# Optimization experiments

Hardware: AMD Instinct MI355X
Metric: run time of the kernel (lower is better)

The kernel has to match this reference:

```python
import jax, jax.numpy as jnp
import numpy as np

HORIZONTAL = 4
VERTICAL = 4


def _laplacian3(x):
    """kornia.filters.laplacian(x, kernel_size=3): 3x3 all-ones kernel with
    center -8, normalized by sum(|k|)=16, reflect padding, depthwise conv.
    x: [B, C, H, W] -> [B, C, H, W]."""
    C = x.shape[1]
    k = np.ones((3, 3), dtype=np.float32)
    k[1, 1] = -8.0
    k /= 16.0  # kornia normalized=True
    kern = jnp.asarray(k, dtype=x.dtype)[None, None].repeat(C, axis=0)  # [C,1,3,3]
    xp = jnp.pad(x, ((0, 0), (0, 0), (1, 1), (1, 1)), mode="reflect")
    return jax.lax.conv_general_dilated(
        xp, kern, window_strides=(1, 1), padding="VALID",
        dimension_numbers=("NCHW", "OIHW", "NCHW"), feature_group_count=C)


def setup_inputs() -> dict:
    key = jax.random.key(0)
    k1, k2 = jax.random.split(key)
    shape = (32, 3, 512, 512)
    return {
        "ground_truth_batch": jax.random.normal(k1, shape, dtype=jnp.float32),
        "segmented_print_batch": jax.random.normal(k2, shape, dtype=jnp.float32),
    }


def reference(ground_truth_batch, segmented_print_batch):
    gt_grad = _laplacian3(ground_truth_batch)
    sp_grad = _laplacian3(segmented_print_batch)
    diff = jnp.abs(gt_grad - sp_grad)  # L1, reduction='sum' per block
    B, C, H, W = diff.shape
    vb, hb = H // VERTICAL, W // HORIZONTAL
    # Original code does image.reshape([H, W, C]) (flat reinterpret), then
    # sums |diff| over [vb, hb, C] blocks of that view. Reproduce exactly:
    d = diff.reshape(B, H, W, C)
    blocks = d.reshape(B, VERTICAL, vb, HORIZONTAL, hb, C).sum(axis=(2, 4, 5))  # [B, V, Hz]
    # Per image, keep the max-loss block; total loss = sum over batch.
    return jnp.max(blocks, axis=(1, 2)).sum()
```

## Files before the change

### kernel.cpp

```cpp
#include <hip/hip_runtime.h>

#define HH 512
#define WW 512
#define CC 3
#define BANDS 8
#define ROWS_PER_BAND 64


__global__ void zero_blocks_kernel(float* __restrict__ blocks, int n) {
    int i = blockIdx.x * blockDim.x + threadIdx.x;
    if (i < n) blocks[i] = 0.0f;
}

__global__ __launch_bounds__(256) void lap_block_sum_kernel(
    const float* __restrict__ gt, const float* __restrict__ sp,
    float* __restrict__ blocks)
{
    __shared__ float ring[4][WW];
    __shared__ float red[4][4];

    const int band = blockIdx.x;
    const int c    = blockIdx.y;
    const int b    = blockIdx.z;
    const int t    = threadIdx.x;
    const int w0   = 2 * t;
    const int w1   = w0 + 1;

    const int h0 = band * ROWS_PER_BAND;
    const size_t plane = (size_t)(b * CC + c) * (size_t)(HH * WW);
    const float* __restrict__ gtp = gt + plane;
    const float* __restrict__ spp = sp + plane;

    auto load_row = [&](int hr) {
        int hs = hr < 0 ? 1 : (hr > HH - 1 ? HH - 2 : hr);
        const float2 g = *(const float2*)(gtp + (size_t)hs * WW + w0);
        const float2 s = *(const float2*)(spp + (size_t)hs * WW + w0);
        float2 d = make_float2(g.x - s.x, g.y - s.y);
        *(float2*)&ring[hr & 3][w0] = d;
    };

    load_row(h0 - 1);
    load_row(h0);

    const int fr0 = c * HH + h0;
    const int v   = fr0 / 384;
    const int hz_m0 = (0 * 512 + w0) / 384;
    const int hz_m1 = (1 * 512 + w0) / 384;
    const int hz_m2 = (2 * 512 + w0) / 384;

    const int wm1 = (w0 == 0)      ? 1      : w0 - 1;
    const int wp2 = (w1 == WW - 1) ? WW - 2 : w1 + 1;

    float acc0 = 0.0f, acc1 = 0.0f, acc2 = 0.0f, acc3 = 0.0f;

    int m = fr0 % 3;
    #pragma unroll 4
    for (int h = h0; h < h0 + ROWS_PER_BAND; ++h) {
        load_row(h + 1);
        __syncthreads();
        const float* __restrict__ r0 = ring[(h - 1) & 3];
        const float* __restrict__ r1 = ring[h & 3];
        const float* __restrict__ r2 = ring[(h + 1) & 3];

        float cm  = r0[wm1] + r1[wm1] + r2[wm1];
        float c0v = r1[w0];
        float cs0 = r0[w0] + c0v + r2[w0];
        float c1v = r1[w1];
        float cs1 = r0[w1] + c1v + r2[w1];
        float cp  = r0[wp2] + r1[wp2] + r2[wp2];

        float lap0 = (cm  + cs0 + cs1 - 9.0f * c0v) * 0.0625f;
        float lap1 = (cs0 + cs1 + cp  - 9.0f * c1v) * 0.0625f;
        float s = fabsf(lap0) + fabsf(lap1);

        int hz = (m == 0) ? hz_m0 : ((m == 1) ? hz_m1 : hz_m2);
        acc0 += (hz == 0) ? s : 0.0f;
        acc1 += (hz == 1) ? s : 0.0f;
        acc2 += (hz == 2) ? s : 0.0f;
        acc3 += (hz == 3) ? s : 0.0f;

        m = (m == 2) ? 0 : m + 1;
    }

    #pragma unroll
    for (int off = 32; off > 0; off >>= 1) {
        acc0 += __shfl_xor(acc0, off);
        acc1 += __shfl_xor(acc1, off);
        acc2 += __shfl_xor(acc2, off);
        acc3 += __shfl_xor(acc3, off);
    }
    const int wave = t >> 6;
    const int lane = t & 63;
    if (lane == 0) {
        red[wave][0] = acc0; red[wave][1] = acc1;
        red[wave][2] = acc2; red[wave][3] = acc3;
    }
    __syncthreads();
    if (t < 4) {
        float r = red[0][t] + red[1][t] + red[2][t] + red[3][t];
        atomicAdd(&blocks[(b * 4 + v) * 4 + t], r);
    }
}

__global__ void finalize_kernel(const float* __restrict__ blocks,
                                float* __restrict__ out, int B) {
    int t = threadIdx.x;
    float m = 0.0f;
    if (t < B) {
        m = blocks[t * 16];
        #pragma unroll
        for (int i = 1; i < 16; ++i) m = fmaxf(m, blocks[t * 16 + i]);
    }
    #pragma unroll
    for (int off = 16; off > 0; off >>= 1) m += __shfl_down(m, off, 32);
    if (t == 0) out[0] = m;
}

extern "C" void kernel_launch(void* const* d_in, const int* in_sizes, int n_in,
                              void* d_out, int out_size, void* d_ws, size_t ws_size,
                              hipStream_t stream) {
    const float* gt = (const float*)d_in[0];
    const float* sp = (const float*)d_in[1];
    float* blocks = (float*)d_ws;
    float* out = (float*)d_out;

    const int B = in_sizes[0] / (CC * HH * WW);

    zero_blocks_kernel<<<1, 512, 0, stream>>>(blocks, B * 16);

    dim3 grid(BANDS, CC, B);
    lap_block_sum_kernel<<<grid, 256, 0, stream>>>(gt, sp, blocks);

    finalize_kernel<<<1, 64, 0, stream>>>(blocks, out, B);
}
```

Baseline: 45.44 us.

## Register-resident stencil with wave-independent row strips and atomic-free partials

Replaces the shared-memory row ring buffer and its per-row __syncthreads with a register sliding window. Each wave owns 8 rows and handles 4-wide columns loaded as float4, with horizontal neighbours fetched by lane shuffles. The grid doubles to 16 bands, and atomics plus the zeroing kernel are replaced by per-workgroup partial sums that a larger finalize kernel reduces. This removes LDS traffic, block-level sync and one launch. In exchange each wave reloads 2 halo rows per 8-row strip and register pressure rises.

Result: slower. 131.0 us (+188.2%).

```diff
diff --git a/kernel.cpp b/kernel.cpp
--- a/kernel.cpp
+++ b/kernel.cpp
@@ -3,84 +3,102 @@
 #define HH 512
 #define WW 512
 #define CC 3
-#define BANDS 8
-#define ROWS_PER_BAND 64
+#define BANDS 16
+#define BAND_ROWS 32
+#define RPW 8
 
 
-__global__ void zero_blocks_kernel(float* __restrict__ blocks, int n) {
-    int i = blockIdx.x * blockDim.x + threadIdx.x;
-    if (i < n) blocks[i] = 0.0f;
-}
-
-__global__ __launch_bounds__(256) void lap_block_sum_kernel(
+__global__ __launch_bounds__(256, 5) void lap_block_sum_kernel(
     const float* __restrict__ gt, const float* __restrict__ sp,
-    float* __restrict__ blocks)
+    float* __restrict__ partial)
 {
-    __shared__ float ring[4][WW];
     __shared__ float red[4][4];
 
-    const int band = blockIdx.x;
-    const int c    = blockIdx.y;
-    const int b    = blockIdx.z;
-    const int t    = threadIdx.x;
-    const int w0   = 2 * t;
-    const int w1   = w0 + 1;
+    const int band = blockIdx.x, c = blockIdx.y, b = blockIdx.z;
+    const int t = threadIdx.x;
+    const int wv = t >> 6, lane = t & 63;
 
-    const int h0 = band * ROWS_PER_BAND;
     const size_t plane = (size_t)(b * CC + c) * (size_t)(HH * WW);
     const float* __restrict__ gtp = gt + plane;
     const float* __restrict__ spp = sp + plane;
 
-    auto load_row = [&](int hr) {
-        int hs = hr < 0 ? 1 : (hr > HH - 1 ? HH - 2 : hr);
-        const float2 g = *(const float2*)(gtp + (size_t)hs * WW + w0);
-        const float2 s = *(const float2*)(spp + (size_t)hs * WW + w0);
-        float2 d = make_float2(g.x - s.x, g.y - s.y);
-        *(float2*)&ring[hr & 3][w0] = d;
-    };
+    const int h0   = band * BAND_ROWS + wv * RPW;
+    const int colA = 4 * lane;
+    const int colB = 256 + 4 * lane;
 
-    load_row(h0 - 1);
-    load_row(h0);
+    const int hzA_0 = (colA) / 384, hzA_1 = (512 + colA) / 384, hzA_2 = (1024 + colA) / 384;
+    const int hzB_0 = (colB) / 384, hzB_1 = (512 + colB) / 384, hzB_2 = (1024 + colB) / 384;
 
-    const int fr0 = c * HH + h0;
-    const int v   = fr0 / 384;
-    const int hz_m0 = (0 * 512 + w0) / 384;
-    const int hz_m1 = (1 * 512 + w0) / 384;
-    const int hz_m2 = (2 * 512 + w0) / 384;
+    float dA[3][4], dB[3][4];
+    float lnA[3], rnA[3], lnB[3], rnB[3];
 
-    const int wm1 = (w0 == 0)      ? 1      : w0 - 1;
-    const int wp2 = (w1 == WW - 1) ? WW - 2 : w1 + 1;
+#define LOAD_ROW(HR, S) do {                                                  \
+        int hs_ = (HR); hs_ = hs_ < 0 ? 1 : (hs_ > HH - 1 ? HH - 2 : hs_);    \
+        const float* gr_ = gtp + (size_t)hs_ * WW;                            \
+        const float* sr_ = spp + (size_t)hs_ * WW;                            \
+        float4 ga_ = *(const float4*)(gr_ + colA);                            \
+        float4 gb_ = *(const float4*)(gr_ + colB);                            \
+        float4 sa_ = *(const float4*)(sr_ + colA);                            \
+        float4 sb_ = *(const float4*)(sr_ + colB);                            \
+        dA[S][0] = ga_.x - sa_.x; dA[S][1] = ga_.y - sa_.y;                   \
+        dA[S][2] = ga_.z - sa_.z; dA[S][3] = ga_.w - sa_.w;                   \
+        dB[S][0] = gb_.x - sb_.x; dB[S][1] = gb_.y - sb_.y;                   \
+        dB[S][2] = gb_.z - sb_.z; dB[S][3] = gb_.w - sb_.w;                   \
+        float lA_  = __shfl(dA[S][3], lane - 1);                              \
+        float rA_  = __shfl(dA[S][0], lane + 1);                              \
+        float lB_  = __shfl(dB[S][3], lane - 1);                              \
+        float rB_  = __shfl(dB[S][0], lane + 1);                              \
+        float xAB_ = __shfl(dB[S][0], 0);      \
+        float xBA_ = __shfl(dA[S][3], 63);      \
+        lnA[S] = (lane == 0)  ? dA[S][1] : lA_;      \
+        rnA[S] = (lane == 63) ? xAB_     : rA_;                               \
+        lnB[S] = (lane == 0)  ? xBA_     : lB_;                               \
+        rnB[S] = (lane == 63) ? dB[S][2] : rB_;   \
+    } while (0)
 
-    float acc0 = 0.0f, acc1 = 0.0f, acc2 = 0.0f, acc3 = 0.0f;
+    LOAD_ROW(h0 - 1, 0);
+    LOAD_ROW(h0,     1);
 
-    int m = fr0 % 3;
-    #pragma unroll 4
-    for (int h = h0; h < h0 + ROWS_PER_BAND; ++h) {
-        load_row(h + 1);
-        __syncthreads();
-        const float* __restrict__ r0 = ring[(h - 1) & 3];
-        const float* __restrict__ r1 = ring[h & 3];
-        const float* __restrict__ r2 = ring[(h + 1) & 3];
+    float acc0 = 0.f, acc1 = 0.f, acc2 = 0.f, acc3 = 0.f;
+    int m = (c * HH + h0) % 3;
 
-        float cm  = r0[wm1] + r1[wm1] + r2[wm1];
-        float c0v = r1[w0];
-        float cs0 = r0[w0] + c0v + r2[w0];
-        float c1v = r1[w1];
-        float cs1 = r0[w1] + c1v + r2[w1];
-        float cp  = r0[wp2] + r1[wp2] + r2[wp2];
+    #pragma unroll
+    for (int i = 0; i < RPW; ++i) {
+        const int sB_ = (i + 2) % 3, sT = i % 3, sM = (i + 1) % 3;
+        LOAD_ROW(h0 + i + 1, sB_);
 
-        float lap0 = (cm  + cs0 + cs1 - 9.0f * c0v) * 0.0625f;
-        float lap1 = (cs0 + cs1 + cp  - 9.0f * c1v) * 0.0625f;
-        float s = fabsf(lap0) + fabsf(lap1);
+        float csA0 = dA[sT][0] + dA[sM][0] + dA[sB_][0];
+        float csA1 = dA[sT][1] + dA[sM][1] + dA[sB_][1];
+        float csA2 = dA[sT][2] + dA[sM][2] + dA[sB_][2];
+        float csA3 = dA[sT][3] + dA[sM][3] + dA[sB_][3];
+        float csLA = lnA[sT] + lnA[sM] + lnA[sB_];
+        float csRA = rnA[sT] + rnA[sM] + rnA[sB_];
+        float sA = fabsf(csLA + csA0 + csA1 - 9.f * dA[sM][0])
+                 + fabsf(csA0 + csA1 + csA2 - 9.f * dA[sM][1])
+                 + fabsf(csA1 + csA2 + csA3 - 9.f * dA[sM][2])
+                 + fabsf(csA2 + csA3 + csRA - 9.f * dA[sM][3]);
 
-        int hz = (m == 0) ? hz_m0 : ((m == 1) ? hz_m1 : hz_m2);
-        acc0 += (hz == 0) ? s : 0.0f;
-        acc1 += (hz == 1) ? s : 0.0f;
-        acc2 += (hz == 2) ? s : 0.0f;
-        acc3 += (hz == 3) ? s : 0.0f;
+        float csB0 = dB[sT][0] + dB[sM][0] + dB[sB_][0];
+        float csB1 = dB[sT][1] + dB[sM][1] + dB[sB_][1];
+        float csB2 = dB[sT][2] + dB[sM][2] + dB[sB_][2];
+        float csB3 = dB[sT][3] + dB[sM][3] + dB[sB_][3];
+        float csLB = lnB[sT] + lnB[sM] + lnB[sB_];
+        float csRB = rnB[sT] + rnB[sM] + rnB[sB_];
+        float sB = fabsf(csLB + csB0 + csB1 - 9.f * dB[sM][0])
+                 + fabsf(csB0 + csB1 + csB2 - 9.f * dB[sM][1])
+                 + fabsf(csB1 + csB2 + csB3 - 9.f * dB[sM][2])
+                 + fabsf(csB2 + csB3 + csRB - 9.f * dB[sM][3]);
 
-        m = (m == 2) ? 0 : m + 1;
+        int hzA = (m == 0) ? hzA_0 : ((m == 1) ? hzA_1 : hzA_2);
+        int hzB = (m == 0) ? hzB_0 : ((m == 1) ? hzB_1 : hzB_2);
+        acc0 += ((hzA == 0) ? sA : 0.f) + ((hzB == 0) ? sB : 0.f);
+        acc1 += ((hzA == 1) ? sA : 0.f) + ((hzB == 1) ? sB : 0.f);
+        acc2 += ((hzA == 2) ? sA : 0.f) + ((hzB == 2) ? sB : 0.f);
+        acc3 += ((hzA == 3) ? sA : 0.f) + ((hzB == 3) ? sB : 0.f);
+
+        m = (m == 2) ? 0 : (m + 1);
     }
+#undef LOAD_ROW
 
     #pragma unroll
     for (int off = 32; off > 0; off >>= 1) {
@@ -89,31 +107,46 @@
         acc2 += __shfl_xor(acc2, off);
         acc3 += __shfl_xor(acc3, off);
     }
-    const int wave = t >> 6;
-    const int lane = t & 63;
     if (lane == 0) {
-        red[wave][0] = acc0; red[wave][1] = acc1;
-        red[wave][2] = acc2; red[wave][3] = acc3;
+        red[wv][0] = acc0 * 0.0625f; red[wv][1] = acc1 * 0.0625f;
+        red[wv][2] = acc2 * 0.0625f; red[wv][3] = acc3 * 0.0625f;
     }
     __syncthreads();
     if (t < 4) {
-        float r = red[0][t] + red[1][t] + red[2][t] + red[3][t];
-        atomicAdd(&blocks[(b * 4 + v) * 4 + t], r);
+        const int wg = band + BANDS * (c + CC * b);
+        partial[wg * 4 + t] = red[0][t] + red[1][t] + red[2][t] + red[3][t];
     }
 }
 
-__global__ void finalize_kernel(const float* __restrict__ blocks,
-                                float* __restrict__ out, int B) {
-    int t = threadIdx.x;
-    float m = 0.0f;
-    if (t < B) {
-        m = blocks[t * 16];
+__global__ void finalize_kernel(const float* __restrict__ partial,
+                                float* __restrict__ out, int B)
+{
+    __shared__ float bmax[32];
+    const int t = threadIdx.x;
+    const int b = t >> 4, v = (t >> 2) & 3, hz = t & 3;
+    float s = 0.f;
+    if (b < B) {
         #pragma unroll
-        for (int i = 1; i < 16; ++i) m = fmaxf(m, blocks[t * 16 + i]);
+        for (int c = 0; c < CC; ++c) {
+            #pragma unroll
+            for (int band = 0; band < BANDS; ++band) {
+                if ((c * HH + band * BAND_ROWS) / 384 == v)
+                    s += partial[(band + BANDS * (c + CC * b)) * 4 + hz];
+            }
+        }
     }
     #pragma unroll
-    for (int off = 16; off > 0; off >>= 1) m += __shfl_down(m, off, 32);
-    if (t == 0) out[0] = m;
+    for (int off = 8; off > 0; off >>= 1)
+        s = fmaxf(s, __shfl_xor(s, off));
+    if ((t & 15) == 0) bmax[b] = (b < B) ? s : 0.f;
+    __syncthreads();
+    if (t < 64) {
+        float x = (t < 32) ? bmax[t] : 0.f;
+        #pragma unroll
+        for (int off = 16; off > 0; off >>= 1)
+            x += __shfl_down(x, off);
+        if (t == 0) out[0] = x;
+    }
 }
 
 extern "C" void kernel_launch(void* const* d_in, const int* in_sizes, int n_in,
@@ -121,15 +154,13 @@
                               hipStream_t stream) {
     const float* gt = (const float*)d_in[0];
     const float* sp = (const float*)d_in[1];
-    float* blocks = (float*)d_ws;
+    float* partial = (float*)d_ws;
     float* out = (float*)d_out;
 
     const int B = in_sizes[0] / (CC * HH * WW);
 
-    zero_blocks_kernel<<<1, 512, 0, stream>>>(blocks, B * 16);
+    dim3 grid(BANDS, CC, B);
+    lap_block_sum_kernel<<<grid, 256, 0, stream>>>(gt, sp, partial);
 
-    dim3 grid(BANDS, CC, B);
-    lap_block_sum_kernel<<<grid, 256, 0, stream>>>(gt, sp, blocks);
-
-    finalize_kernel<<<1, 64, 0, stream>>>(blocks, out, B);
+    finalize_kernel<<<1, 512, 0, stream>>>(partial, out, B);
 }
```
